# Kernel optimization log

Measured on AMD Instinct MI355X. Metric: run time of the kernel, lower is better.

## Reference

```python
import jax, jax.numpy as jnp
import numpy as np

EPS = 1e-5
TOP_K = 2

def _conv(x, w, pad):
    # x: [B,Cin,H,W], w: [Cout,Cin,kh,kw]
    return jax.lax.conv_general_dilated(
        x, w, (1, 1), [(pad, pad), (pad, pad)],
        dimension_numbers=('NCHW', 'OIHW', 'NCHW'))

def _bn_eval(x, scale, bias):
    # BatchNorm2d in eval mode with running_mean=0, running_var=1
    inv = scale / jnp.sqrt(1.0 + EPS)
    return x * inv[None, :, None, None] + bias[None, :, None, None]

def setup_inputs() -> dict:
    key = jax.random.key(0)
    ks = jax.random.split(key, 8)
    B, C, O, H, W, E, HID = 16, 256, 256, 56, 56, 8, 512  # HID = int(2.0 * C)
    g = lambda k, shape, f: jax.random.normal(k, shape, jnp.float32) * f
    return {
        'x': jax.random.normal(ks[0], (B, C, H, W), jnp.float32),
        # EfficientSpatialRouter: global-avg-pool -> 1x1 conv to E logits
        'router_w': g(ks[1], (E, C), 0.01),
        'router_b': jnp.zeros((E,), jnp.float32),
        # shared expert: 1x1 conv -> BN -> SiLU
        'shared_w': g(ks[2], (O, C, 1, 1), 0.05),
        'shared_scale': jnp.ones((O,), jnp.float32),
        'shared_bias': jnp.zeros((O,), jnp.float32),
        # SimpleExpert per expert: conv3x3 C->HID, BN, SiLU, conv1x1 HID->O, BN
        'w1': g(ks[3], (E, HID, C, 3, 3), 0.02),
        'bn1_scale': jnp.ones((E, HID), jnp.float32),
        'bn1_bias': jnp.zeros((E, HID), jnp.float32),
        'w2': g(ks[4], (E, O, HID, 1, 1), 0.02),
        'bn2_scale': jnp.ones((E, O), jnp.float32),
        'bn2_bias': jnp.zeros((E, O), jnp.float32),
    }

def reference(x, router_w, router_b, shared_w, shared_scale, shared_bias,
              w1, bn1_scale, bn1_bias, w2, bn2_scale, bn2_bias):
    E = router_w.shape[0]
    # --- routing: pooled features -> logits -> softmax -> top-k renormalized ---
    pooled = x.mean(axis=(2, 3))                          # [B,C]
    logits = pooled @ router_w.T + router_b               # [B,E]
    probs = jax.nn.softmax(logits, axis=-1)
    topk_vals, topk_idx = jax.lax.top_k(probs, TOP_K)     # [B,K]
    weights = topk_vals / topk_vals.sum(axis=-1, keepdims=True)
    # --- shared expert ---
    shared = jax.nn.silu(_bn_eval(_conv(x, shared_w, 0), shared_scale, shared_bias))
    # --- expert dispatch/combine (dense-masked equivalent of gather + index_add) ---
    expert_out = jnp.zeros_like(shared)
    for e in range(E):  # fixed small expert count
        gate = jnp.sum(weights * (topk_idx == e), axis=-1)  # [B], 0 if not routed
        h = jax.nn.silu(_bn_eval(_conv(x, w1[e], 1), bn1_scale[e], bn1_bias[e]))
        y = _bn_eval(_conv(h, w2[e], 0), bn2_scale[e], bn2_bias[e])
        expert_out = expert_out + gate[:, None, None, None] * y
    # residual since in_channels == out_channels
    return shared + expert_out + x
```

## Files before the change

### kernel.cpp

```cpp
#include <hip/hip_runtime.h>
#include <hip/hip_bf16.h>

#define B_ 16
#define C_ 256
#define O_ 256
#define P_ 3136
#define E_ 8
#define HID_ 512
#define EPS_ 1e-5f

typedef __attribute__((ext_vector_type(8))) short bf16x8;
typedef __attribute__((ext_vector_type(4))) float f32x4;
typedef __hip_bfloat16 bf16;

__device__ __forceinline__ void gl2lds16(const bf16* g, bf16* l) {
  __builtin_amdgcn_global_load_lds((const __attribute__((address_space(1))) void*)g,
                                   (__attribute__((address_space(3))) void*)l,
                                   16, 0, 0);
}

__device__ __forceinline__ f32x4 mfma16(bf16x8 a, bf16x8 b, f32x4 c) {
  return __builtin_amdgcn_mfma_f32_16x16x32_bf16(a, b, c, 0, 0, 0);
}

__global__ __launch_bounds__(256) void xT_kernel(const float* __restrict__ x,
                                                 bf16* __restrict__ xT,
                                                 float* __restrict__ pooled) {
  __shared__ float tile[64][65];
  const int p0 = blockIdx.x * 64, c0 = blockIdx.y * 64, b = blockIdx.z;
  const int t = threadIdx.x;
#pragma unroll
  for (int j = 0; j < 16; ++j) {
    int idx = t + j * 256;
    int cl = idx >> 6, pl = idx & 63;
    tile[cl][pl] = x[(size_t)(b * C_ + c0 + cl) * P_ + p0 + pl];
  }
  __syncthreads();
#pragma unroll
  for (int j = 0; j < 16; ++j) {
    int idx = t + j * 256;
    int pl = idx >> 6, cl = idx & 63;
    xT[(size_t)(b * P_ + p0 + pl) * C_ + c0 + cl] = __float2bfloat16(tile[cl][pl]);
  }
  if (t < 64) {
    float s = 0.f;
#pragma unroll 8
    for (int pl = 0; pl < 64; ++pl) s += tile[t][pl];
    atomicAdd(&pooled[b * C_ + c0 + t], s * (1.0f / P_));
  }
}

__global__ __launch_bounds__(256) void w1cvt_kernel(const float* __restrict__ w1,
                                                    const float* __restrict__ bn1_scale,
                                                    bf16* __restrict__ w1b) {
  const int eh = blockIdx.x;
  const int e = eh >> 9, hid = eh & 511;
  __shared__ float buf[2304];
  const float* src = w1 + (size_t)eh * 2304;
  const int t = threadIdx.x;
  for (int i = t; i < 2304; i += 256) buf[i] = src[i];
  __syncthreads();
  const float inv = bn1_scale[eh] * (1.0f / sqrtf(1.0f + EPS_));
  for (int i = t; i < 2304; i += 256) {
    int rs = i >> 8, c = i & 255;
    w1b[((size_t)(e * 9 + rs) * HID_ + hid) * C_ + c] = __float2bfloat16(buf[c * 9 + rs] * inv);
  }
}

__global__ __launch_bounds__(256) void w2cvt_kernel(const float* __restrict__ w2,
                                                    const float* __restrict__ bn2_scale,
                                                    bf16* __restrict__ w2b) {
  const int i = blockIdx.x * 256 + threadIdx.x;
  const int eo = i >> 9;
  w2b[i] = __float2bfloat16(w2[i] * (bn2_scale[eo] * (1.0f / sqrtf(1.0f + EPS_))));
}

__global__ __launch_bounds__(256) void wshcvt_kernel(const float* __restrict__ wsh,
                                                     const float* __restrict__ sscale,
                                                     bf16* __restrict__ wshb) {
  const int i = blockIdx.x * 256 + threadIdx.x;
  wshb[i] = __float2bfloat16(wsh[i] * (sscale[i >> 8] * (1.0f / sqrtf(1.0f + EPS_))));
}

__global__ __launch_bounds__(256) void router_kernel(const float* __restrict__ pooled,
                                                     const float* __restrict__ rw,
                                                     const float* __restrict__ rb,
                                                     const float* __restrict__ bn2_bias,
                                                     int* __restrict__ ridx,
                                                     float* __restrict__ rwt,
                                                     float* __restrict__ bsum) {
  __shared__ float lp[B_ * C_];
  __shared__ float llog[B_ * E_];
  __shared__ int lidx[B_ * 2];
  __shared__ float lw[B_ * 2];
  const int t = threadIdx.x;
  for (int i = t; i < B_ * C_; i += 256) lp[i] = pooled[i];
  __syncthreads();
  if (t < B_ * E_) {
    int b = t >> 3, e = t & 7;
    float s = rb[e];
    for (int c = 0; c < C_; ++c) s += lp[b * C_ + c] * rw[e * C_ + c];
    llog[t] = s;
  }
  __syncthreads();
  if (t < B_) {
    float pr[E_];
    float m = -1e30f;
    for (int e = 0; e < E_; ++e) { pr[e] = llog[t * E_ + e]; m = fmaxf(m, pr[e]); }
    float s = 0.f;
    for (int e = 0; e < E_; ++e) { pr[e] = __expf(pr[e] - m); s += pr[e]; }
    const float is = 1.f / s;
    for (int e = 0; e < E_; ++e) pr[e] *= is;
    int i0 = 0; float v0 = pr[0];
    for (int e = 1; e < E_; ++e) if (pr[e] > v0) { v0 = pr[e]; i0 = e; }
    int i1 = -1; float v1 = -1.f;
    for (int e = 0; e < E_; ++e) if (e != i0 && pr[e] > v1) { v1 = pr[e]; i1 = e; }
    const float wsum = 1.f / (v0 + v1);
    ridx[t * 2] = i0; ridx[t * 2 + 1] = i1;
    rwt[t * 2] = v0 * wsum; rwt[t * 2 + 1] = v1 * wsum;
    lidx[t * 2] = i0; lidx[t * 2 + 1] = i1;
    lw[t * 2] = v0 * wsum; lw[t * 2 + 1] = v1 * wsum;
  }
  __syncthreads();
  for (int i = t; i < B_ * O_; i += 256) {
    int b = i >> 8, o = i & 255;
    bsum[i] = lw[b * 2] * bn2_bias[lidx[b * 2] * O_ + o]
            + lw[b * 2 + 1] * bn2_bias[lidx[b * 2 + 1] * O_ + o];
  }
}

__global__ __launch_bounds__(512, 2) void conv1_kernel(
    const bf16* __restrict__ xT, const bf16* __restrict__ w1b,
    const float* __restrict__ bn1_bias, const int* __restrict__ ridx,
    const float* __restrict__ rwt, const bf16* __restrict__ zp,
    bf16* __restrict__ h) {
  __shared__ __align__(16) bf16 ldsA[3][256 * 64];
  __shared__ __align__(16) bf16 ldsB[3][128 * 64];
  const int t = threadIdx.x;
  const int bid = blockIdx.x;
  const int xcd = bid & 7, j = bid >> 3;
  const int bsl = j / 52, tile = j % 52;
  const int mt = tile % 13, nt = tile / 13;
  const int bs = xcd * 4 + bsl;
  const int p0 = mt * 256, h0 = nt * 128;
  const int b = bs >> 1;
  const int e = ridx[bs];
  const float wk = rwt[bs];

  const int lane = t & 63, wv = t >> 6;
  const int wm = wv >> 1, wn = wv & 1;
  const int r16 = lane & 15, q = lane >> 4;

  const int srow = t >> 3;
  const int cho = ((t & 7) ^ (srow & 7)) * 8;
  int pA[4], yA[4], xA[4];
#pragma unroll
  for (int r = 0; r < 4; ++r) {
    pA[r] = p0 + r * 64 + srow;
    yA[r] = pA[r] / 56;
    xA[r] = pA[r] - yA[r] * 56;
  }
  const bf16* xb = xT + (size_t)b * P_ * C_ + cho;
  const bf16* wb = w1b + ((size_t)(e * 9) * HID_ + h0 + srow) * C_ + cho;
  bf16* laT = &ldsA[0][0] + t * 8;
  bf16* lbT = &ldsB[0][0] + t * 8;

  auto STAGE = [&](int bf, int s) {
    const int tap = s >> 2, ck = (s & 3) * 64;
    const int dr = tap / 3 - 1, dc = tap % 3 - 1;
    const int off = dr * 56 + dc;
#pragma unroll
    for (int r = 0; r < 4; ++r) {
      const bool v = (pA[r] < P_) & ((unsigned)(yA[r] + dr) < 56u) & ((unsigned)(xA[r] + dc) < 56u);
      const bf16* sp = v ? xb + (size_t)(pA[r] + off) * C_ + ck : zp;
      gl2lds16(sp, laT + bf * 16384 + r * 4096);
    }
    const bf16* wsrc = wb + (size_t)tap * HID_ * C_ + ck;
    gl2lds16(wsrc, lbT + bf * 8192);
    gl2lds16(wsrc + 64 * C_, lbT + bf * 8192 + 4096);
  };

  f32x4 acc[4][4] = {};

  STAGE(0, 0);
  STAGE(1, 1);
  asm volatile("s_waitcnt vmcnt(6)" ::: "memory");
  __builtin_amdgcn_s_barrier();
  asm volatile("" ::: "memory");

  const int Abase = (wm * 64 + r16) * 64;
  const int Bbase = (wn * 64 + r16) * 64;
  const int sb0 = (q ^ (r16 & 7)) * 8;
  const int sb1 = ((4 + q) ^ (r16 & 7)) * 8;
  int cb = 0;
  for (int kt = 0; kt < 36; ++kt) {
    if (kt < 34) {
      const int nbf = cb + 2 >= 3 ? cb - 1 : cb + 2;
      STAGE(nbf, kt + 2);
    }
    const bf16* lA = &ldsA[0][0] + cb * 16384;
    const bf16* lB = &ldsB[0][0] + cb * 8192;
    bf16x8 a0[4], a1[4], b0v[4], b1v[4];
#pragma unroll
    for (int i = 0; i < 4; ++i) {
      a0[i] = *(const bf16x8*)(lA + Abase + i * 1024 + sb0);
      a1[i] = *(const bf16x8*)(lA + Abase + i * 1024 + sb1);
      b0v[i] = *(const bf16x8*)(lB + Bbase + i * 1024 + sb0);
      b1v[i] = *(const bf16x8*)(lB + Bbase + i * 1024 + sb1);
    }
    __builtin_amdgcn_s_setprio(1);
#pragma unroll
    for (int mi = 0; mi < 4; ++mi)
#pragma unroll
      for (int ni = 0; ni < 4; ++ni) {
        acc[mi][ni] = mfma16(a0[mi], b0v[ni], acc[mi][ni]);
        acc[mi][ni] = mfma16(a1[mi], b1v[ni], acc[mi][ni]);
      }
    __builtin_amdgcn_s_setprio(0);
    if (kt < 35) {
      if (kt < 34) asm volatile("s_waitcnt vmcnt(6)" ::: "memory");
      else         asm volatile("s_waitcnt vmcnt(0)" ::: "memory");
      __builtin_amdgcn_s_barrier();
      asm volatile("" ::: "memory");
    }
    cb = cb + 1 >= 3 ? 0 : cb + 1;
  }

  const int rowq = q * 4;
  float bias[4];
#pragma unroll
  for (int ni = 0; ni < 4; ++ni)
    bias[ni] = bn1_bias[e * HID_ + h0 + wn * 64 + ni * 16 + r16];
#pragma unroll
  for (int mi = 0; mi < 4; ++mi) {
#pragma unroll
    for (int i = 0; i < 4; ++i) {
      const int p = p0 + wm * 64 + mi * 16 + rowq + i;
      if (p < P_) {
        const size_t base = ((size_t)bs * P_ + p) * HID_;
#pragma unroll
        for (int ni = 0; ni < 4; ++ni) {
          const int hid = h0 + wn * 64 + ni * 16 + r16;
          float v = acc[mi][ni][i] + bias[ni];
          v = v / (1.f + __expf(-v));
          h[base + hid] = __float2bfloat16(wk * v);
        }
      }
    }
  }
}

__global__ __launch_bounds__(512, 2) void combine_kernel(
    const bf16* __restrict__ xT, const bf16* __restrict__ h,
    const bf16* __restrict__ wshb, const bf16* __restrict__ w2b,
    const float* __restrict__ sbias, const float* __restrict__ bsum,
    const int* __restrict__ ridx, const float* __restrict__ x,
    const bf16* __restrict__ zp, float* __restrict__ out) {
  __shared__ __align__(16) bf16 ldsA[3][256 * 64];
  __shared__ __align__(16) bf16 ldsB[3][128 * 64];
  const int t = threadIdx.x;
  const int bid = blockIdx.x;
  const int xcd = bid & 7, j = bid >> 3;
  const int bl = j / 25, pt = j % 25;
  const int b = xcd * 2 + bl;
  const int p0 = pt * 128;
  const int e0 = ridx[b * 2], e1 = ridx[b * 2 + 1];

  const int lane = t & 63, wv = t >> 6;
  const int wm = wv >> 1, wn = wv & 1;
  const int r16 = lane & 15, q = lane >> 4;

  const int srow = t >> 3;
  const int cho = ((t & 7) ^ (srow & 7)) * 8;
  int pB[2];
  pB[0] = p0 + srow;
  pB[1] = p0 + 64 + srow;
  const bf16* wshp = wshb + (size_t)srow * C_ + cho;
  const bf16* w2p0 = w2b + ((size_t)(e0 * O_) + srow) * HID_ + cho;
  const bf16* w2p1 = w2b + ((size_t)(e1 * O_) + srow) * HID_ + cho;
  const bf16* xp = xT + (size_t)b * P_ * C_ + cho;
  const bf16* hp0 = h + (size_t)(b * 2) * P_ * HID_ + cho;
  const bf16* hp1 = h + (size_t)(b * 2 + 1) * P_ * HID_ + cho;
  bf16* laT = &ldsA[0][0] + t * 8;
  bf16* lbT = &ldsB[0][0] + t * 8;

  auto CSTAGE = [&](int bf, int s) {
    if (s < 4) {
      const int ck = s * 64;
#pragma unroll
      for (int r = 0; r < 4; ++r)
        gl2lds16(wshp + (size_t)(r * 64) * C_ + ck, laT + bf * 16384 + r * 4096);
#pragma unroll
      for (int r = 0; r < 2; ++r) {
        const bf16* sp = (pB[r] < P_) ? xp + (size_t)pB[r] * C_ + ck : zp;
        gl2lds16(sp, lbT + bf * 8192 + r * 4096);
      }
    } else {
      const int ss = s - 4;
      const int sl = ss >> 3, ck = (ss & 7) * 64;
      const bf16* wa = sl ? w2p1 : w2p0;
      const bf16* hb = sl ? hp1 : hp0;
#pragma unroll
      for (int r = 0; r < 4; ++r)
        gl2lds16(wa + (size_t)(r * 64) * HID_ + ck, laT + bf * 16384 + r * 4096);
#pragma unroll
      for (int r = 0; r < 2; ++r) {
        const bf16* sp = (pB[r] < P_) ? hb + (size_t)pB[r] * HID_ + ck : zp;
        gl2lds16(sp, lbT + bf * 8192 + r * 4096);
      }
    }
  };

  const int rowq = q * 4;
  float sb_[4][4];
#pragma unroll
  for (int mi = 0; mi < 4; ++mi)
#pragma unroll
    for (int i = 0; i < 4; ++i)
      sb_[mi][i] = sbias[wm * 64 + mi * 16 + rowq + i];

  f32x4 acc[4][4] = {};

  CSTAGE(0, 0);
  CSTAGE(1, 1);
  asm volatile("s_waitcnt vmcnt(6)" ::: "memory");
  __builtin_amdgcn_s_barrier();
  asm volatile("" ::: "memory");

  const int Abase = (wm * 64 + r16) * 64;
  const int Bbase = (wn * 64 + r16) * 64;
  const int sb0 = (q ^ (r16 & 7)) * 8;
  const int sb1 = ((4 + q) ^ (r16 & 7)) * 8;
  int cb = 0;
  for (int kt = 0; kt < 20; ++kt) {
    if (kt < 18) {
      const int nbf = cb + 2 >= 3 ? cb - 1 : cb + 2;
      CSTAGE(nbf, kt + 2);
    }
    const bf16* lA = &ldsA[0][0] + cb * 16384;
    const bf16* lB = &ldsB[0][0] + cb * 8192;
    bf16x8 a0[4], a1[4], b0v[4], b1v[4];
#pragma unroll
    for (int i = 0; i < 4; ++i) {
      a0[i] = *(const bf16x8*)(lA + Abase + i * 1024 + sb0);
      a1[i] = *(const bf16x8*)(lA + Abase + i * 1024 + sb1);
      b0v[i] = *(const bf16x8*)(lB + Bbase + i * 1024 + sb0);
      b1v[i] = *(const bf16x8*)(lB + Bbase + i * 1024 + sb1);
    }
    __builtin_amdgcn_s_setprio(1);
#pragma unroll
    for (int mi = 0; mi < 4; ++mi)
#pragma unroll
      for (int ni = 0; ni < 4; ++ni) {
        acc[mi][ni] = mfma16(a0[mi], b0v[ni], acc[mi][ni]);
        acc[mi][ni] = mfma16(a1[mi], b1v[ni], acc[mi][ni]);
      }
    __builtin_amdgcn_s_setprio(0);
    if (kt == 3) {
#pragma unroll
      for (int mi = 0; mi < 4; ++mi)
#pragma unroll
        for (int i = 0; i < 4; ++i)
#pragma unroll
          for (int ni = 0; ni < 4; ++ni) {
            float v = acc[mi][ni][i] + sb_[mi][i];
            acc[mi][ni][i] = v / (1.f + __expf(-v));
          }
    }
    if (kt < 19) {
      if (kt < 18) asm volatile("s_waitcnt vmcnt(6)" ::: "memory");
      else         asm volatile("s_waitcnt vmcnt(0)" ::: "memory");
      __builtin_amdgcn_s_barrier();
      asm volatile("" ::: "memory");
    }
    cb = cb + 1 >= 3 ? 0 : cb + 1;
  }

#pragma unroll
  for (int mi = 0; mi < 4; ++mi) {
#pragma unroll
    for (int i = 0; i < 4; ++i) {
      const int o = wm * 64 + mi * 16 + rowq + i;
      const float bb = bsum[b * O_ + o];
      const size_t orow = (size_t)(b * O_ + o) * P_;
#pragma unroll
      for (int ni = 0; ni < 4; ++ni) {
        const int p = p0 + wn * 64 + ni * 16 + r16;
        if (p < P_) out[orow + p] = acc[mi][ni][i] + bb + x[orow + p];
      }
    }
  }
}

constexpr size_t SZ_XT = (size_t)B_ * P_ * C_ * 2;
constexpr size_t SZ_W1B = (size_t)E_ * 9 * HID_ * C_ * 2;
constexpr size_t SZ_W2B = (size_t)E_ * O_ * HID_ * 2;
constexpr size_t SZ_WSHB = (size_t)O_ * C_ * 2;
constexpr size_t SZ_POOL = (size_t)B_ * C_ * 4;
constexpr size_t SZ_BSUM = (size_t)B_ * O_ * 4;

constexpr size_t OFF_XT = 0;
constexpr size_t OFF_W1B = OFF_XT + SZ_XT;
constexpr size_t OFF_W2B = OFF_W1B + SZ_W1B;
constexpr size_t OFF_WSHB = OFF_W2B + SZ_W2B;
constexpr size_t OFF_POOL = OFF_WSHB + SZ_WSHB;
constexpr size_t OFF_RIDX = OFF_POOL + SZ_POOL;
constexpr size_t OFF_RWT = OFF_RIDX + 128;
constexpr size_t OFF_BSUM = OFF_RWT + 128;
constexpr size_t OFF_ZERO = OFF_BSUM + SZ_BSUM;
constexpr size_t OFF_H = OFF_ZERO + 1024;

extern "C" void kernel_launch(void* const* d_in, const int* in_sizes, int n_in,
                              void* d_out, int out_size, void* d_ws, size_t ws_size,
                              hipStream_t stream) {
  const float* x = (const float*)d_in[0];
  const float* router_w = (const float*)d_in[1];
  const float* router_b = (const float*)d_in[2];
  const float* shared_w = (const float*)d_in[3];
  const float* shared_scale = (const float*)d_in[4];
  const float* shared_bias = (const float*)d_in[5];
  const float* w1 = (const float*)d_in[6];
  const float* bn1_scale = (const float*)d_in[7];
  const float* bn1_bias = (const float*)d_in[8];
  const float* w2 = (const float*)d_in[9];
  const float* bn2_scale = (const float*)d_in[10];
  const float* bn2_bias = (const float*)d_in[11];
  float* out = (float*)d_out;
  char* ws = (char*)d_ws;

  bf16* xT = (bf16*)(ws + OFF_XT);
  bf16* w1b = (bf16*)(ws + OFF_W1B);
  bf16* w2b = (bf16*)(ws + OFF_W2B);
  bf16* wshb = (bf16*)(ws + OFF_WSHB);
  float* pooled = (float*)(ws + OFF_POOL);
  int* ridx = (int*)(ws + OFF_RIDX);
  float* rwt = (float*)(ws + OFF_RWT);
  float* bsum = (float*)(ws + OFF_BSUM);
  bf16* zp = (bf16*)(ws + OFF_ZERO);
  bf16* h = (bf16*)(ws + OFF_H);

  hipMemsetAsync(ws + OFF_POOL, 0, SZ_POOL, stream);
  hipMemsetAsync(ws + OFF_ZERO, 0, 1024, stream);

  xT_kernel<<<dim3(49, 4, 16), 256, 0, stream>>>(x, xT, pooled);
  w1cvt_kernel<<<E_ * HID_, 256, 0, stream>>>(w1, bn1_scale, w1b);
  w2cvt_kernel<<<(E_ * O_ * HID_) / 256, 256, 0, stream>>>(w2, bn2_scale, w2b);
  wshcvt_kernel<<<(O_ * C_) / 256, 256, 0, stream>>>(shared_w, shared_scale, wshb);
  router_kernel<<<1, 256, 0, stream>>>(pooled, router_w, router_b, bn2_bias, ridx, rwt, bsum);
  conv1_kernel<<<1664, 512, 0, stream>>>(xT, w1b, bn1_bias, ridx, rwt, zp, h);
  combine_kernel<<<400, 512, 0, stream>>>(xT, h, wshb, w2b, shared_bias, bsum, ridx, x, zp, out);
}
```

Baseline: 628.9 us.

## Shrink conv1 and combine GEMM tiles to 128x128 with K=32 stages and 256 threads

Both GEMM kernels change from 512-thread blocks with 256x128 (or 256-row) tiles and K=64 stages to 256-thread blocks with 128x128 tiles and K=32 stages. The LDS swizzle and the staging code are rewritten to match, and the combine kernel now also splits the output-channel dimension. The goal is more blocks (3200 and 800), smaller LDS use and higher occupancy, with better load balance across CUs. In exchange there are twice as many barrier-synchronised iterations, and each tile gets less operand reuse, which raises global and LDS traffic per FLOP.

```diff
diff --git a/kernel.cpp b/kernel.cpp
--- a/kernel.cpp
+++ b/kernel.cpp
@@ -129,20 +129,20 @@
   }
 }
 
-__global__ __launch_bounds__(512, 2) void conv1_kernel(
+__global__ __launch_bounds__(256, 3) void conv1_kernel(
     const bf16* __restrict__ xT, const bf16* __restrict__ w1b,
     const float* __restrict__ bn1_bias, const int* __restrict__ ridx,
     const float* __restrict__ rwt, const bf16* __restrict__ zp,
     bf16* __restrict__ h) {
-  __shared__ __align__(16) bf16 ldsA[3][256 * 64];
-  __shared__ __align__(16) bf16 ldsB[3][128 * 64];
+  __shared__ __align__(16) bf16 ldsA[3][4096];
+  __shared__ __align__(16) bf16 ldsB[3][4096];
   const int t = threadIdx.x;
   const int bid = blockIdx.x;
   const int xcd = bid & 7, j = bid >> 3;
-  const int bsl = j / 52, tile = j % 52;
-  const int mt = tile % 13, nt = tile / 13;
+  const int bsl = j / 100, j2 = j % 100;
+  const int mt = j2 % 25, nt = j2 / 25;
   const int bs = xcd * 4 + bsl;
-  const int p0 = mt * 256, h0 = nt * 128;
+  const int p0 = mt * 128, h0 = nt * 128;
   const int b = bs >> 1;
   const int e = ridx[bs];
   const float wk = rwt[bs];
@@ -150,75 +150,65 @@
   const int lane = t & 63, wv = t >> 6;
   const int wm = wv >> 1, wn = wv & 1;
   const int r16 = lane & 15, q = lane >> 4;
-
-  const int srow = t >> 3;
-  const int cho = ((t & 7) ^ (srow & 7)) * 8;
-  int pA[4], yA[4], xA[4];
-#pragma unroll
-  for (int r = 0; r < 4; ++r) {
-    pA[r] = p0 + r * 64 + srow;
-    yA[r] = pA[r] / 56;
-    xA[r] = pA[r] - yA[r] * 56;
-  }
+  const int koffA = ((q ^ ((r16 >> 1) & 3)) * 8);
+
+  const int srow = t >> 2;
+  const int cho = (((t & 3) ^ ((srow >> 1) & 3)) * 8);
+  const int pA0 = p0 + srow, pA1 = pA0 + 64;
+  const int yA0 = pA0 / 56, xA0 = pA0 - yA0 * 56;
+  const int yA1 = pA1 / 56, xA1 = pA1 - yA1 * 56;
   const bf16* xb = xT + (size_t)b * P_ * C_ + cho;
   const bf16* wb = w1b + ((size_t)(e * 9) * HID_ + h0 + srow) * C_ + cho;
   bf16* laT = &ldsA[0][0] + t * 8;
   bf16* lbT = &ldsB[0][0] + t * 8;
 
   auto STAGE = [&](int bf, int s) {
-    const int tap = s >> 2, ck = (s & 3) * 64;
-    const int dr = tap / 3 - 1, dc = tap % 3 - 1;
+    const int tap = s >> 3, ck = (s & 7) * 32;
+    const int dr = ((tap * 11) >> 5) - 1;
+    const int dc = tap - (dr + 1) * 3 - 1;
     const int off = dr * 56 + dc;
-#pragma unroll
-    for (int r = 0; r < 4; ++r) {
-      const bool v = (pA[r] < P_) & ((unsigned)(yA[r] + dr) < 56u) & ((unsigned)(xA[r] + dc) < 56u);
-      const bf16* sp = v ? xb + (size_t)(pA[r] + off) * C_ + ck : zp;
-      gl2lds16(sp, laT + bf * 16384 + r * 4096);
-    }
-    const bf16* wsrc = wb + (size_t)tap * HID_ * C_ + ck;
-    gl2lds16(wsrc, lbT + bf * 8192);
-    gl2lds16(wsrc + 64 * C_, lbT + bf * 8192 + 4096);
+    const bool v0 = (pA0 < P_) & ((unsigned)(yA0 + dr) < 56u) & ((unsigned)(xA0 + dc) < 56u);
+    const bool v1 = (pA1 < P_) & ((unsigned)(yA1 + dr) < 56u) & ((unsigned)(xA1 + dc) < 56u);
+    gl2lds16(v0 ? xb + (size_t)(pA0 + off) * C_ + ck : zp, laT + bf * 4096);
+    gl2lds16(v1 ? xb + (size_t)(pA1 + off) * C_ + ck : zp, laT + bf * 4096 + 2048);
+    const bf16* wsrc = wb + (size_t)tap * (HID_ * C_) + ck;
+    gl2lds16(wsrc, lbT + bf * 4096);
+    gl2lds16(wsrc + 64 * C_, lbT + bf * 4096 + 2048);
   };
 
   f32x4 acc[4][4] = {};
 
   STAGE(0, 0);
   STAGE(1, 1);
-  asm volatile("s_waitcnt vmcnt(6)" ::: "memory");
+  asm volatile("s_waitcnt vmcnt(4)" ::: "memory");
   __builtin_amdgcn_s_barrier();
   asm volatile("" ::: "memory");
 
-  const int Abase = (wm * 64 + r16) * 64;
-  const int Bbase = (wn * 64 + r16) * 64;
-  const int sb0 = (q ^ (r16 & 7)) * 8;
-  const int sb1 = ((4 + q) ^ (r16 & 7)) * 8;
+  const int Abase = (wm * 64 + r16) * 32 + koffA;
+  const int Bbase = (wn * 64 + r16) * 32 + koffA;
   int cb = 0;
-  for (int kt = 0; kt < 36; ++kt) {
-    if (kt < 34) {
+  for (int kt = 0; kt < 72; ++kt) {
+    if (kt < 70) {
       const int nbf = cb + 2 >= 3 ? cb - 1 : cb + 2;
       STAGE(nbf, kt + 2);
     }
-    const bf16* lA = &ldsA[0][0] + cb * 16384;
-    const bf16* lB = &ldsB[0][0] + cb * 8192;
-    bf16x8 a0[4], a1[4], b0v[4], b1v[4];
+    const bf16* lA = &ldsA[0][0] + cb * 4096;
+    const bf16* lB = &ldsB[0][0] + cb * 4096;
+    bf16x8 af[4], bf[4];
 #pragma unroll
     for (int i = 0; i < 4; ++i) {
-      a0[i] = *(const bf16x8*)(lA + Abase + i * 1024 + sb0);
-      a1[i] = *(const bf16x8*)(lA + Abase + i * 1024 + sb1);
-      b0v[i] = *(const bf16x8*)(lB + Bbase + i * 1024 + sb0);
-      b1v[i] = *(const bf16x8*)(lB + Bbase + i * 1024 + sb1);
+      af[i] = *(const bf16x8*)(lA + Abase + i * 512);
+      bf[i] = *(const bf16x8*)(lB + Bbase + i * 512);
     }
     __builtin_amdgcn_s_setprio(1);
 #pragma unroll
     for (int mi = 0; mi < 4; ++mi)
 #pragma unroll
-      for (int ni = 0; ni < 4; ++ni) {
-        acc[mi][ni] = mfma16(a0[mi], b0v[ni], acc[mi][ni]);
-        acc[mi][ni] = mfma16(a1[mi], b1v[ni], acc[mi][ni]);
-      }
+      for (int ni = 0; ni < 4; ++ni)
+        acc[mi][ni] = mfma16(af[mi], bf[ni], acc[mi][ni]);
     __builtin_amdgcn_s_setprio(0);
-    if (kt < 35) {
-      if (kt < 34) asm volatile("s_waitcnt vmcnt(6)" ::: "memory");
+    if (kt < 71) {
+      if (kt < 70) asm volatile("s_waitcnt vmcnt(4)" ::: "memory");
       else         asm volatile("s_waitcnt vmcnt(0)" ::: "memory");
       __builtin_amdgcn_s_barrier();
       asm volatile("" ::: "memory");
@@ -250,34 +240,35 @@
   }
 }
 
-__global__ __launch_bounds__(512, 2) void combine_kernel(
+__global__ __launch_bounds__(256, 3) void combine_kernel(
     const bf16* __restrict__ xT, const bf16* __restrict__ h,
     const bf16* __restrict__ wshb, const bf16* __restrict__ w2b,
     const float* __restrict__ sbias, const float* __restrict__ bsum,
     const int* __restrict__ ridx, const float* __restrict__ x,
     const bf16* __restrict__ zp, float* __restrict__ out) {
-  __shared__ __align__(16) bf16 ldsA[3][256 * 64];
-  __shared__ __align__(16) bf16 ldsB[3][128 * 64];
+  __shared__ __align__(16) bf16 ldsA[3][4096];
+  __shared__ __align__(16) bf16 ldsB[3][4096];
   const int t = threadIdx.x;
   const int bid = blockIdx.x;
   const int xcd = bid & 7, j = bid >> 3;
-  const int bl = j / 25, pt = j % 25;
+  const int bl = j / 50, j2 = j % 50;
+  const int ot = j2 / 25, pt = j2 % 25;
   const int b = xcd * 2 + bl;
-  const int p0 = pt * 128;
+  const int o0 = ot * 128, p0 = pt * 128;
   const int e0 = ridx[b * 2], e1 = ridx[b * 2 + 1];
 
   const int lane = t & 63, wv = t >> 6;
   const int wm = wv >> 1, wn = wv & 1;
   const int r16 = lane & 15, q = lane >> 4;
-
-  const int srow = t >> 3;
-  const int cho = ((t & 7) ^ (srow & 7)) * 8;
-  int pB[2];
-  pB[0] = p0 + srow;
-  pB[1] = p0 + 64 + srow;
-  const bf16* wshp = wshb + (size_t)srow * C_ + cho;
-  const bf16* w2p0 = w2b + ((size_t)(e0 * O_) + srow) * HID_ + cho;
-  const bf16* w2p1 = w2b + ((size_t)(e1 * O_) + srow) * HID_ + cho;
+  const int koffA = ((q ^ ((r16 >> 1) & 3)) * 8);
+
+  const int srow = t >> 2;
+  const int cho = (((t & 3) ^ ((srow >> 1) & 3)) * 8);
+  const int pB0 = p0 + srow, pB1 = pB0 + 64;
+  const bool vB0 = (pB0 < P_), vB1 = (pB1 < P_);
+  const bf16* wshp = wshb + (size_t)(o0 + srow) * C_ + cho;
+  const bf16* w2p0 = w2b + ((size_t)(e0 * O_) + o0 + srow) * HID_ + cho;
+  const bf16* w2p1 = w2b + ((size_t)(e1 * O_) + o0 + srow) * HID_ + cho;
   const bf16* xp = xT + (size_t)b * P_ * C_ + cho;
   const bf16* hp0 = h + (size_t)(b * 2) * P_ * HID_ + cho;
   const bf16* hp1 = h + (size_t)(b * 2 + 1) * P_ * HID_ + cho;
@@ -285,30 +276,27 @@
   bf16* lbT = &ldsB[0][0] + t * 8;
 
   auto CSTAGE = [&](int bf, int s) {
-    if (s < 4) {
-      const int ck = s * 64;
-#pragma unroll
-      for (int r = 0; r < 4; ++r)
-        gl2lds16(wshp + (size_t)(r * 64) * C_ + ck, laT + bf * 16384 + r * 4096);
-#pragma unroll
-      for (int r = 0; r < 2; ++r) {
-        const bf16* sp = (pB[r] < P_) ? xp + (size_t)pB[r] * C_ + ck : zp;
-        gl2lds16(sp, lbT + bf * 8192 + r * 4096);
-      }
+    const bf16 *a0, *a1, *b0, *b1;
+    if (s < 8) {
+      const int ck = s * 32;
+      a0 = wshp + ck;
+      a1 = wshp + 64 * C_ + ck;
+      b0 = vB0 ? xp + (size_t)pB0 * C_ + ck : zp;
+      b1 = vB1 ? xp + (size_t)pB1 * C_ + ck : zp;
     } else {
-      const int ss = s - 4;
-      const int sl = ss >> 3, ck = (ss & 7) * 64;
+      const int ss = s - 8;
+      const int sl = ss >> 4, ck = (ss & 15) * 32;
       const bf16* wa = sl ? w2p1 : w2p0;
       const bf16* hb = sl ? hp1 : hp0;
-#pragma unroll
-      for (int r = 0; r < 4; ++r)
-        gl2lds16(wa + (size_t)(r * 64) * HID_ + ck, laT + bf * 16384 + r * 4096);
-#pragma unroll
-      for (int r = 0; r < 2; ++r) {
-        const bf16* sp = (pB[r] < P_) ? hb + (size_t)pB[r] * HID_ + ck : zp;
-        gl2lds16(sp, lbT + bf * 8192 + r * 4096);
-      }
-    }
+      a0 = wa + ck;
+      a1 = wa + 64 * HID_ + ck;
+      b0 = vB0 ? hb + (size_t)pB0 * HID_ + ck : zp;
+      b1 = vB1 ? hb + (size_t)pB1 * HID_ + ck : zp;
+    }
+    gl2lds16(a0, laT + bf * 4096);
+    gl2lds16(a1, laT + bf * 4096 + 2048);
+    gl2lds16(b0, lbT + bf * 4096);
+    gl2lds16(b1, lbT + bf * 4096 + 2048);
   };
 
   const int rowq = q * 4;
@@ -317,46 +305,40 @@
   for (int mi = 0; mi < 4; ++mi)
 #pragma unroll
     for (int i = 0; i < 4; ++i)
-      sb_[mi][i] = sbias[wm * 64 + mi * 16 + rowq + i];
+      sb_[mi][i] = sbias[o0 + wm * 64 + mi * 16 + rowq + i];
 
   f32x4 acc[4][4] = {};
 
   CSTAGE(0, 0);
   CSTAGE(1, 1);
-  asm volatile("s_waitcnt vmcnt(6)" ::: "memory");
+  asm volatile("s_waitcnt vmcnt(4)" ::: "memory");
   __builtin_amdgcn_s_barrier();
   asm volatile("" ::: "memory");
 
-  const int Abase = (wm * 64 + r16) * 64;
-  const int Bbase = (wn * 64 + r16) * 64;
-  const int sb0 = (q ^ (r16 & 7)) * 8;
-  const int sb1 = ((4 + q) ^ (r16 & 7)) * 8;
+  const int Abase = (wm * 64 + r16) * 32 + koffA;
+  const int Bbase = (wn * 64 + r16) * 32 + koffA;
   int cb = 0;
-  for (int kt = 0; kt < 20; ++kt) {
-    if (kt < 18) {
+  for (int kt = 0; kt < 40; ++kt) {
+    if (kt < 38) {
       const int nbf = cb + 2 >= 3 ? cb - 1 : cb + 2;
       CSTAGE(nbf, kt + 2);
     }
-    const bf16* lA = &ldsA[0][0] + cb * 16384;
-    const bf16* lB = &ldsB[0][0] + cb * 8192;
-    bf16x8 a0[4], a1[4], b0v[4], b1v[4];
+    const bf16* lA = &ldsA[0][0] + cb * 4096;
+    const bf16* lB = &ldsB[0][0] + cb * 4096;
+    bf16x8 af[4], bf[4];
 #pragma unroll
     for (int i = 0; i < 4; ++i) {
-      a0[i] = *(const bf16x8*)(lA + Abase + i * 1024 + sb0);
-      a1[i] = *(const bf16x8*)(lA + Abase + i * 1024 + sb1);
-      b0v[i] = *(const bf16x8*)(lB + Bbase + i * 1024 + sb0);
-      b1v[i] = *(const bf16x8*)(lB + Bbase + i * 1024 + sb1);
+      af[i] = *(const bf16x8*)(lA + Abase + i * 512);
+      bf[i] = *(const bf16x8*)(lB + Bbase + i * 512);
     }
     __builtin_amdgcn_s_setprio(1);
 #pragma unroll
     for (int mi = 0; mi < 4; ++mi)
 #pragma unroll
-      for (int ni = 0; ni < 4; ++ni) {
-        acc[mi][ni] = mfma16(a0[mi], b0v[ni], acc[mi][ni]);
-        acc[mi][ni] = mfma16(a1[mi], b1v[ni], acc[mi][ni]);
-      }
+      for (int ni = 0; ni < 4; ++ni)
+        acc[mi][ni] = mfma16(af[mi], bf[ni], acc[mi][ni]);
     __builtin_amdgcn_s_setprio(0);
-    if (kt == 3) {
+    if (kt == 7) {
 #pragma unroll
       for (int mi = 0; mi < 4; ++mi)
 #pragma unroll
@@ -367,8 +349,8 @@
             acc[mi][ni][i] = v / (1.f + __expf(-v));
           }
     }
-    if (kt < 19) {
-      if (kt < 18) asm volatile("s_waitcnt vmcnt(6)" ::: "memory");
+    if (kt < 39) {
+      if (kt < 38) asm volatile("s_waitcnt vmcnt(4)" ::: "memory");
       else         asm volatile("s_waitcnt vmcnt(0)" ::: "memory");
       __builtin_amdgcn_s_barrier();
       asm volatile("" ::: "memory");
@@ -380,7 +362,7 @@
   for (int mi = 0; mi < 4; ++mi) {
 #pragma unroll
     for (int i = 0; i < 4; ++i) {
-      const int o = wm * 64 + mi * 16 + rowq + i;
+      const int o = o0 + wm * 64 + mi * 16 + rowq + i;
       const float bb = bsum[b * O_ + o];
       const size_t orow = (size_t)(b * O_ + o) * P_;
 #pragma unroll
@@ -447,6 +429,6 @@
   w2cvt_kernel<<<(E_ * O_ * HID_) / 256, 256, 0, stream>>>(w2, bn2_scale, w2b);
   wshcvt_kernel<<<(O_ * C_) / 256, 256, 0, stream>>>(shared_w, shared_scale, wshb);
   router_kernel<<<1, 256, 0, stream>>>(pooled, router_w, router_b, bn2_bias, ridx, rwt, bsum);
-  conv1_kernel<<<1664, 512, 0, stream>>>(xT, w1b, bn1_bias, ridx, rwt, zp, h);
-  combine_kernel<<<400, 512, 0, stream>>>(xT, h, wshb, w2b, shared_bias, bsum, ridx, x, zp, out);
-}
+  conv1_kernel<<<3200, 256, 0, stream>>>(xT, w1b, bn1_bias, ridx, rwt, zp, h);
+  combine_kernel<<<800, 256, 0, stream>>>(xT, h, wshb, w2b, shared_bias, bsum, ridx, x, zp, out);
+}
```

Result: faster. 592.9 us (-5.7%).
